# Optimization experiments

Hardware: AMD Instinct MI355X
Metric: run time of the kernel (lower is better)

Reference implementation:

```python
import jax, jax.numpy as jnp
import numpy as np

N_FALSE_NEG = 64
TEMPERATURE = 0.1
NORMALIZE = True

B, T, D = 32, 512, 512
M = 4096


def setup_inputs() -> dict:
    key = jax.random.key(0)
    k1, k2, k3 = jax.random.split(key, 3)
    input_predicted = jax.random.normal(k1, (B, T, D), dtype=jnp.float32)
    input_encoded = jax.random.normal(k2, (B, T, D), dtype=jnp.float32)
    rows = jax.random.randint(k3, (M,), 0, B)
    cols = jax.random.randint(jax.random.fold_in(k3, 1), (M,), 0, T)
    mask_ids = jnp.stack([rows, cols], axis=1).astype(jnp.int64)
    return {"input_predicted": input_predicted, "input_encoded": input_encoded, "mask_ids": mask_ids}


def _l2norm(x, eps=1e-12):
    # matches F.normalize(p=2, dim=-1)
    n = jnp.sqrt(jnp.sum(x * x, axis=-1, keepdims=True))
    return x / jnp.maximum(n, eps)


def reference(input_predicted, input_encoded, mask_ids):
    m = mask_ids.shape[0]
    rows, cols = mask_ids[:, 0], mask_ids[:, 1]
    enc = input_encoded[rows, cols]      # [M, D] encoded at masked positions
    preds = input_predicted[rows, cols]  # [M, D]

    # negatives_from_same_seq_only=False branch:
    # candidates = arange(0, M-1); idx_pos = i; torch.randint(0, M-2) -> [0, M-3]
    r = jax.random.randint(jax.random.key(42), (m, N_FALSE_NEG), 0, m - 2)  # [M, K]
    i = jnp.arange(m)[:, None]
    sel = r + (r >= i).astype(r.dtype)   # skip the positive index
    negatives = enc[sel]                 # [M, K, D]

    candidates = jnp.concatenate([enc[:, None, :], negatives], axis=1)  # [M, K+1, D]
    if NORMALIZE:
        candidates = _l2norm(candidates)
        preds = _l2norm(preds)

    sim = jnp.einsum('md,mcd->mc', preds, candidates) / TEMPERATURE  # [M, K+1]
    # cross entropy with target class 0
    lse = jax.nn.logsumexp(sim, axis=-1)
    loss = jnp.mean(lse - sim[:, 0])
    acc = jnp.mean((jnp.argmax(sim, axis=-1) == 0).astype(jnp.float32))
    return loss, acc
```

## Files before the change

kernel.cpp:

```cpp
#include <hip/hip_runtime.h>
#include <stdint.h>

#define T_DIM 512
#define D_DIM 512
#define M_ROWS 4096
#define NNEG 64
#define INV_TEMP 10.0f
#define SPAN 4094u
#define MULT 1024u

typedef float v2f __attribute__((ext_vector_type(2)));

struct U2 { uint32_t a, b; };

__host__ __device__ constexpr uint32_t rotl32(uint32_t x, uint32_t r) {
  return (x << r) | (x >> (32u - r));
}

__host__ __device__ constexpr U2 tf2x32(uint32_t k0, uint32_t k1,
                                        uint32_t c0, uint32_t c1) {
  uint32_t ks0 = k0, ks1 = k1, ks2 = k0 ^ k1 ^ 0x1BD11BDAu;
  uint32_t x0 = c0 + ks0, x1 = c1 + ks1;
  x0 += x1; x1 = rotl32(x1, 13); x1 ^= x0;
  x0 += x1; x1 = rotl32(x1, 15); x1 ^= x0;
  x0 += x1; x1 = rotl32(x1, 26); x1 ^= x0;
  x0 += x1; x1 = rotl32(x1, 6);  x1 ^= x0;
  x0 += ks1; x1 += ks2 + 1u;
  x0 += x1; x1 = rotl32(x1, 17); x1 ^= x0;
  x0 += x1; x1 = rotl32(x1, 29); x1 ^= x0;
  x0 += x1; x1 = rotl32(x1, 16); x1 ^= x0;
  x0 += x1; x1 = rotl32(x1, 24); x1 ^= x0;
  x0 += ks2; x1 += ks0 + 2u;
  x0 += x1; x1 = rotl32(x1, 13); x1 ^= x0;
  x0 += x1; x1 = rotl32(x1, 15); x1 ^= x0;
  x0 += x1; x1 = rotl32(x1, 26); x1 ^= x0;
  x0 += x1; x1 = rotl32(x1, 6);  x1 ^= x0;
  x0 += ks0; x1 += ks1 + 3u;
  x0 += x1; x1 = rotl32(x1, 17); x1 ^= x0;
  x0 += x1; x1 = rotl32(x1, 29); x1 ^= x0;
  x0 += x1; x1 = rotl32(x1, 16); x1 ^= x0;
  x0 += x1; x1 = rotl32(x1, 24); x1 ^= x0;
  x0 += ks1; x1 += ks2 + 4u;
  x0 += x1; x1 = rotl32(x1, 13); x1 ^= x0;
  x0 += x1; x1 = rotl32(x1, 15); x1 ^= x0;
  x0 += x1; x1 = rotl32(x1, 26); x1 ^= x0;
  x0 += x1; x1 = rotl32(x1, 6);  x1 ^= x0;
  x0 += ks2; x1 += ks0 + 5u;
  return U2{x0, x1};
}

constexpr U2 KHI = tf2x32(0u, 42u, 0u, 0u);
constexpr U2 KLO = tf2x32(0u, 42u, 0u, 1u);

__device__ inline uint32_t sel_index(uint32_t m, uint32_t j) {
  uint32_t pos = m * 64u + j;
  U2 h = tf2x32(KHI.a, KHI.b, 0u, pos);
  U2 l = tf2x32(KLO.a, KLO.b, 0u, pos);
  uint32_t hi = h.a ^ h.b;
  uint32_t lo = l.a ^ l.b;
  uint32_t r = ((hi % SPAN) * MULT + (lo % SPAN)) % SPAN;
  return r + (r >= m ? 1u : 0u);
}

__global__ __launch_bounds__(256) void k_norm_enc(
    const float* __restrict__ enc, const int* __restrict__ ids,
    int2* __restrict__ nenc) {
  int lane = threadIdx.x & 63;
  int wave = threadIdx.x >> 6;
  int m = blockIdx.x * 4 + wave;

  int2 rc = ((const int2*)ids)[m];
  size_t base = ((size_t)rc.x * T_DIM + rc.y) * D_DIM;
  const float4* ep = (const float4*)(enc + base);
  float4 e0 = ep[2 * lane], e1 = ep[2 * lane + 1];

  float se = e0.x*e0.x + e0.y*e0.y + e0.z*e0.z + e0.w*e0.w
           + e1.x*e1.x + e1.y*e1.y + e1.z*e1.z + e1.w*e1.w;
  #pragma unroll
  for (int off = 1; off < 64; off <<= 1) se += __shfl_xor(se, off, 64);
  float inv_e = 1.0f / fmaxf(sqrtf(se), 1e-12f);

  int w0 = __builtin_amdgcn_cvt_pk_fp8_f32(e0.x * inv_e, e0.y * inv_e, 0, false);
  w0     = __builtin_amdgcn_cvt_pk_fp8_f32(e0.z * inv_e, e0.w * inv_e, w0, true);
  int w1 = __builtin_amdgcn_cvt_pk_fp8_f32(e1.x * inv_e, e1.y * inv_e, 0, false);
  w1     = __builtin_amdgcn_cvt_pk_fp8_f32(e1.z * inv_e, e1.w * inv_e, w1, true);
  nenc[m * 64 + lane] = make_int2(w0, w1);
}

__device__ inline float dot8_fp8(int2 q, const float* pn) {
  v2f a = __builtin_amdgcn_cvt_pk_f32_fp8(q.x, false);
  float d = pn[0] * a.x;
  d = fmaf(pn[1], a.y, d);
  a = __builtin_amdgcn_cvt_pk_f32_fp8(q.x, true);
  d = fmaf(pn[2], a.x, d); d = fmaf(pn[3], a.y, d);
  a = __builtin_amdgcn_cvt_pk_f32_fp8(q.y, false);
  d = fmaf(pn[4], a.x, d); d = fmaf(pn[5], a.y, d);
  a = __builtin_amdgcn_cvt_pk_f32_fp8(q.y, true);
  d = fmaf(pn[6], a.x, d); d = fmaf(pn[7], a.y, d);
  return d;
}

__global__ __launch_bounds__(256) void k_contrast(
    const float* __restrict__ pred, const int* __restrict__ ids,
    const int2* __restrict__ nenc, float2* __restrict__ partials) {
  int lane = threadIdx.x & 63;
  int wave = threadIdx.x >> 6;
  int m = blockIdx.x * 4 + wave;

  __shared__ int sel_lds[4][64];
  __shared__ float2 wred[4];
  sel_lds[wave][lane] = (int)sel_index((uint32_t)m, (uint32_t)lane);

  int2 rc = ((const int2*)ids)[m];
  size_t base = ((size_t)rc.x * T_DIM + rc.y) * D_DIM;
  const float4* pp = (const float4*)(pred + base);
  float4 p0 = pp[2 * lane], p1 = pp[2 * lane + 1];
  float sp = p0.x*p0.x + p0.y*p0.y + p0.z*p0.z + p0.w*p0.w
           + p1.x*p1.x + p1.y*p1.y + p1.z*p1.z + p1.w*p1.w;
  #pragma unroll
  for (int off = 1; off < 64; off <<= 1) sp += __shfl_xor(sp, off, 64);
  float inv_p = 1.0f / fmaxf(sqrtf(sp), 1e-12f);

  float pn[8];
  pn[0] = p0.x*inv_p; pn[1] = p0.y*inv_p; pn[2] = p0.z*inv_p; pn[3] = p0.w*inv_p;
  pn[4] = p1.x*inv_p; pn[5] = p1.y*inv_p; pn[6] = p1.z*inv_p; pn[7] = p1.w*inv_p;

  float dp = dot8_fp8(nenc[m * 64 + lane], pn);
  #pragma unroll
  for (int off = 1; off < 64; off <<= 1) dp += __shfl_xor(dp, off, 64);
  float s0 = dp * INV_TEMP;

  float sumexp = __expf(s0);
  float maxneg = -1e30f;

  for (int jj = 0; jj < NNEG; jj += 4) {
    int4 s4 = *((const int4*)&sel_lds[wave][jj]);
    int2 q0 = nenc[(size_t)s4.x * 64 + lane];
    int2 q1 = nenc[(size_t)s4.y * 64 + lane];
    int2 q2 = nenc[(size_t)s4.z * 64 + lane];
    int2 q3 = nenc[(size_t)s4.w * 64 + lane];
    float d0 = dot8_fp8(q0, pn);
    float d1 = dot8_fp8(q1, pn);
    float d2 = dot8_fp8(q2, pn);
    float d3 = dot8_fp8(q3, pn);
    #pragma unroll
    for (int off = 1; off < 64; off <<= 1) {
      d0 += __shfl_xor(d0, off, 64);
      d1 += __shfl_xor(d1, off, 64);
      d2 += __shfl_xor(d2, off, 64);
      d3 += __shfl_xor(d3, off, 64);
    }
    float s_0 = d0 * INV_TEMP, s_1 = d1 * INV_TEMP;
    float s_2 = d2 * INV_TEMP, s_3 = d3 * INV_TEMP;
    maxneg = fmaxf(fmaxf(fmaxf(maxneg, s_0), fmaxf(s_1, s_2)), s_3);
    sumexp += __expf(s_0) + __expf(s_1) + __expf(s_2) + __expf(s_3);
  }

  if (lane == 0) {
    float lse = logf(sumexp);
    wred[wave] = make_float2(lse - s0, (s0 >= maxneg) ? 1.0f : 0.0f);
  }
  __syncthreads();
  if (threadIdx.x == 0) {
    float l = 0.0f, a = 0.0f;
    #pragma unroll
    for (int w = 0; w < 4; ++w) { l += wred[w].x; a += wred[w].y; }
    partials[blockIdx.x] = make_float2(l, a);
  }
}

__global__ __launch_bounds__(256) void k_finalize(
    const float2* __restrict__ partials, float* __restrict__ out) {
  int t = threadIdx.x;
  float l = 0.0f, a = 0.0f;
  #pragma unroll
  for (int i = 0; i < 4; ++i) {
    float2 v = partials[t + 256 * i];
    l += v.x; a += v.y;
  }
  #pragma unroll
  for (int off = 1; off < 64; off <<= 1) {
    l += __shfl_xor(l, off, 64);
    a += __shfl_xor(a, off, 64);
  }
  __shared__ float2 wred[4];
  if ((t & 63) == 0) wred[t >> 6] = make_float2(l, a);
  __syncthreads();
  if (t == 0) {
    out[0] = (wred[0].x + wred[1].x + wred[2].x + wred[3].x) * (1.0f / M_ROWS);
    out[1] = (wred[0].y + wred[1].y + wred[2].y + wred[3].y) * (1.0f / M_ROWS);
  }
}

extern "C" void kernel_launch(void* const* d_in, const int* in_sizes, int n_in,
                              void* d_out, int out_size, void* d_ws, size_t ws_size,
                              hipStream_t stream) {
  const float* pred = (const float*)d_in[0];
  const float* enc  = (const float*)d_in[1];
  const int*   ids  = (const int*)d_in[2];
  float* out = (float*)d_out;

  int2* nenc = (int2*)d_ws;
  float2* partials = (float2*)(nenc + (size_t)M_ROWS * 64);

  k_norm_enc<<<M_ROWS / 4, 256, 0, stream>>>(enc, ids, nenc);
  k_contrast<<<M_ROWS / 4, 256, 0, stream>>>(pred, ids, nenc, partials);
  k_finalize<<<1, 256, 0, stream>>>(partials, out);
}
```

Measured before the change: 115.1 us.

## Precompute negative indices, vectorize fp8 dots, quad-split reductions, fuse finalize via atomics

The Threefry negative-index generation moves into the normalization kernel and is written to a workspace table, so the contrast kernel only loads it. The fp8 dot product uses packed v2f FMAs. The per-negative 64-lane reductions are replaced by a scheme where four candidates share one butterfly, with each 16-lane quad finishing one candidate. The separate finalize kernel is removed: blocks accumulate float atomics and the last block writes the output. This removes one launch and cuts shuffle and hash ALU work, at the cost of nondeterministic float atomic ordering and a counter reset that depends on kernel ordering.

```diff
diff --git a/kernel.cpp b/kernel.cpp
--- a/kernel.cpp
+++ b/kernel.cpp
@@ -8,6 +8,7 @@
 #define INV_TEMP 10.0f
 #define SPAN 4094u
 #define MULT 1024u
+#define NBLK (M_ROWS / 4)
 
 typedef float v2f __attribute__((ext_vector_type(2)));
 
@@ -64,10 +65,15 @@
 
 __global__ __launch_bounds__(256) void k_norm_enc(
     const float* __restrict__ enc, const int* __restrict__ ids,
-    int2* __restrict__ nenc) {
+    int2* __restrict__ nenc, int* __restrict__ selTab,
+    unsigned int* __restrict__ accum) {
   int lane = threadIdx.x & 63;
   int wave = threadIdx.x >> 6;
   int m = blockIdx.x * 4 + wave;
+
+  if (blockIdx.x == 0 && threadIdx.x < 4) accum[threadIdx.x] = 0u;
+
+  selTab[m * 64 + lane] = (int)sel_index((uint32_t)m, (uint32_t)lane);
 
   int2 rc = ((const int2*)ids)[m];
   size_t base = ((size_t)rc.x * T_DIM + rc.y) * D_DIM;
@@ -87,29 +93,43 @@
   nenc[m * 64 + lane] = make_int2(w0, w1);
 }
 
-__device__ inline float dot8_fp8(int2 q, const float* pn) {
-  v2f a = __builtin_amdgcn_cvt_pk_f32_fp8(q.x, false);
-  float d = pn[0] * a.x;
-  d = fmaf(pn[1], a.y, d);
-  a = __builtin_amdgcn_cvt_pk_f32_fp8(q.x, true);
-  d = fmaf(pn[2], a.x, d); d = fmaf(pn[3], a.y, d);
-  a = __builtin_amdgcn_cvt_pk_f32_fp8(q.y, false);
-  d = fmaf(pn[4], a.x, d); d = fmaf(pn[5], a.y, d);
-  a = __builtin_amdgcn_cvt_pk_f32_fp8(q.y, true);
-  d = fmaf(pn[6], a.x, d); d = fmaf(pn[7], a.y, d);
-  return d;
+__device__ inline float dot8_fp8v(int2 q, const v2f* pn2) {
+  v2f a0 = __builtin_amdgcn_cvt_pk_f32_fp8(q.x, false);
+  v2f acc = a0 * pn2[0];
+  v2f a1 = __builtin_amdgcn_cvt_pk_f32_fp8(q.x, true);
+  acc = __builtin_elementwise_fma(a1, pn2[1], acc);
+  v2f a2 = __builtin_amdgcn_cvt_pk_f32_fp8(q.y, false);
+  acc = __builtin_elementwise_fma(a2, pn2[2], acc);
+  v2f a3 = __builtin_amdgcn_cvt_pk_f32_fp8(q.y, true);
+  acc = __builtin_elementwise_fma(a3, pn2[3], acc);
+  return acc.x + acc.y;
+}
+
+__device__ inline float reduce4(float d0, float d1, float d2, float d3, int quad) {
+  d0 += __shfl_xor(d0, 16, 64); d0 += __shfl_xor(d0, 32, 64);
+  d1 += __shfl_xor(d1, 16, 64); d1 += __shfl_xor(d1, 32, 64);
+  d2 += __shfl_xor(d2, 16, 64); d2 += __shfl_xor(d2, 32, 64);
+  d3 += __shfl_xor(d3, 16, 64); d3 += __shfl_xor(d3, 32, 64);
+  float c = (quad == 0) ? d0 : (quad == 1) ? d1 : (quad == 2) ? d2 : d3;
+  c += __shfl_xor(c, 1, 64);
+  c += __shfl_xor(c, 2, 64);
+  c += __shfl_xor(c, 4, 64);
+  c += __shfl_xor(c, 8, 64);
+  return c;
 }
 
 __global__ __launch_bounds__(256) void k_contrast(
     const float* __restrict__ pred, const int* __restrict__ ids,
-    const int2* __restrict__ nenc, float2* __restrict__ partials) {
+    const int2* __restrict__ nenc, const int* __restrict__ selTab,
+    unsigned int* __restrict__ accum, float* __restrict__ out) {
   int lane = threadIdx.x & 63;
   int wave = threadIdx.x >> 6;
   int m = blockIdx.x * 4 + wave;
+  int quad = lane >> 4;
 
   __shared__ int sel_lds[4][64];
   __shared__ float2 wred[4];
-  sel_lds[wave][lane] = (int)sel_index((uint32_t)m, (uint32_t)lane);
+  sel_lds[wave][lane] = selTab[m * 64 + lane];
 
   int2 rc = ((const int2*)ids)[m];
   size_t base = ((size_t)rc.x * T_DIM + rc.y) * D_DIM;
@@ -121,43 +141,47 @@
   for (int off = 1; off < 64; off <<= 1) sp += __shfl_xor(sp, off, 64);
   float inv_p = 1.0f / fmaxf(sqrtf(sp), 1e-12f);
 
-  float pn[8];
-  pn[0] = p0.x*inv_p; pn[1] = p0.y*inv_p; pn[2] = p0.z*inv_p; pn[3] = p0.w*inv_p;
-  pn[4] = p1.x*inv_p; pn[5] = p1.y*inv_p; pn[6] = p1.z*inv_p; pn[7] = p1.w*inv_p;
-
-  float dp = dot8_fp8(nenc[m * 64 + lane], pn);
+  v2f pn2[4];
+  pn2[0] = (v2f){p0.x * inv_p, p0.y * inv_p};
+  pn2[1] = (v2f){p0.z * inv_p, p0.w * inv_p};
+  pn2[2] = (v2f){p1.x * inv_p, p1.y * inv_p};
+  pn2[3] = (v2f){p1.z * inv_p, p1.w * inv_p};
+
+  float dp = dot8_fp8v(nenc[m * 64 + lane], pn2);
   #pragma unroll
   for (int off = 1; off < 64; off <<= 1) dp += __shfl_xor(dp, off, 64);
   float s0 = dp * INV_TEMP;
 
-  float sumexp = __expf(s0);
+  float sumexp_n = 0.0f;
   float maxneg = -1e30f;
 
-  for (int jj = 0; jj < NNEG; jj += 4) {
-    int4 s4 = *((const int4*)&sel_lds[wave][jj]);
-    int2 q0 = nenc[(size_t)s4.x * 64 + lane];
-    int2 q1 = nenc[(size_t)s4.y * 64 + lane];
-    int2 q2 = nenc[(size_t)s4.z * 64 + lane];
-    int2 q3 = nenc[(size_t)s4.w * 64 + lane];
-    float d0 = dot8_fp8(q0, pn);
-    float d1 = dot8_fp8(q1, pn);
-    float d2 = dot8_fp8(q2, pn);
-    float d3 = dot8_fp8(q3, pn);
-    #pragma unroll
-    for (int off = 1; off < 64; off <<= 1) {
-      d0 += __shfl_xor(d0, off, 64);
-      d1 += __shfl_xor(d1, off, 64);
-      d2 += __shfl_xor(d2, off, 64);
-      d3 += __shfl_xor(d3, off, 64);
-    }
-    float s_0 = d0 * INV_TEMP, s_1 = d1 * INV_TEMP;
-    float s_2 = d2 * INV_TEMP, s_3 = d3 * INV_TEMP;
-    maxneg = fmaxf(fmaxf(fmaxf(maxneg, s_0), fmaxf(s_1, s_2)), s_3);
-    sumexp += __expf(s_0) + __expf(s_1) + __expf(s_2) + __expf(s_3);
+  for (int jj = 0; jj < NNEG; jj += 8) {
+    int4 sa = *((const int4*)&sel_lds[wave][jj]);
+    int4 sb = *((const int4*)&sel_lds[wave][jj + 4]);
+    int2 q0 = nenc[(size_t)sa.x * 64 + lane];
+    int2 q1 = nenc[(size_t)sa.y * 64 + lane];
+    int2 q2 = nenc[(size_t)sa.z * 64 + lane];
+    int2 q3 = nenc[(size_t)sa.w * 64 + lane];
+    int2 q4 = nenc[(size_t)sb.x * 64 + lane];
+    int2 q5 = nenc[(size_t)sb.y * 64 + lane];
+    int2 q6 = nenc[(size_t)sb.z * 64 + lane];
+    int2 q7 = nenc[(size_t)sb.w * 64 + lane];
+    float d0 = dot8_fp8v(q0, pn2), d1 = dot8_fp8v(q1, pn2);
+    float d2 = dot8_fp8v(q2, pn2), d3 = dot8_fp8v(q3, pn2);
+    float d4 = dot8_fp8v(q4, pn2), d5 = dot8_fp8v(q5, pn2);
+    float d6 = dot8_fp8v(q6, pn2), d7 = dot8_fp8v(q7, pn2);
+    float c1 = reduce4(d0, d1, d2, d3, quad) * INV_TEMP;
+    float c2 = reduce4(d4, d5, d6, d7, quad) * INV_TEMP;
+    maxneg = fmaxf(maxneg, fmaxf(c1, c2));
+    sumexp_n += __expf(c1) + __expf(c2);
   }
+  sumexp_n += __shfl_xor(sumexp_n, 16, 64);
+  sumexp_n += __shfl_xor(sumexp_n, 32, 64);
+  maxneg = fmaxf(maxneg, __shfl_xor(maxneg, 16, 64));
+  maxneg = fmaxf(maxneg, __shfl_xor(maxneg, 32, 64));
 
   if (lane == 0) {
-    float lse = logf(sumexp);
+    float lse = logf(sumexp_n + __expf(s0));
     wred[wave] = make_float2(lse - s0, (s0 >= maxneg) ? 1.0f : 0.0f);
   }
   __syncthreads();
@@ -165,30 +189,17 @@
     float l = 0.0f, a = 0.0f;
     #pragma unroll
     for (int w = 0; w < 4; ++w) { l += wred[w].x; a += wred[w].y; }
-    partials[blockIdx.x] = make_float2(l, a);
-  }
-}
-
-__global__ __launch_bounds__(256) void k_finalize(
-    const float2* __restrict__ partials, float* __restrict__ out) {
-  int t = threadIdx.x;
-  float l = 0.0f, a = 0.0f;
-  #pragma unroll
-  for (int i = 0; i < 4; ++i) {
-    float2 v = partials[t + 256 * i];
-    l += v.x; a += v.y;
-  }
-  #pragma unroll
-  for (int off = 1; off < 64; off <<= 1) {
-    l += __shfl_xor(l, off, 64);
-    a += __shfl_xor(a, off, 64);
-  }
-  __shared__ float2 wred[4];
-  if ((t & 63) == 0) wred[t >> 6] = make_float2(l, a);
-  __syncthreads();
-  if (t == 0) {
-    out[0] = (wred[0].x + wred[1].x + wred[2].x + wred[3].x) * (1.0f / M_ROWS);
-    out[1] = (wred[0].y + wred[1].y + wred[2].y + wred[3].y) * (1.0f / M_ROWS);
+    float* facc = (float*)accum;
+    atomicAdd(&facc[0], l);
+    atomicAdd(&facc[1], a);
+    __threadfence();
+    unsigned int old = atomicAdd(&accum[2], 1u);
+    if (old == NBLK - 1) {
+      float ll = atomicAdd(&facc[0], 0.0f);
+      float aa = atomicAdd(&facc[1], 0.0f);
+      out[0] = ll * (1.0f / M_ROWS);
+      out[1] = aa * (1.0f / M_ROWS);
+    }
   }
 }
 
@@ -201,9 +212,9 @@
   float* out = (float*)d_out;
 
   int2* nenc = (int2*)d_ws;
-  float2* partials = (float2*)(nenc + (size_t)M_ROWS * 64);
-
-  k_norm_enc<<<M_ROWS / 4, 256, 0, stream>>>(enc, ids, nenc);
-  k_contrast<<<M_ROWS / 4, 256, 0, stream>>>(pred, ids, nenc, partials);
-  k_finalize<<<1, 256, 0, stream>>>(partials, out);
-}
+  int* selTab = (int*)(nenc + (size_t)M_ROWS * 64);
+  unsigned int* accum = (unsigned int*)(selTab + (size_t)M_ROWS * 64);
+
+  k_norm_enc<<<NBLK, 256, 0, stream>>>(enc, ids, nenc, selTab, accum);
+  k_contrast<<<NBLK, 256, 0, stream>>>(pred, ids, nenc, selTab, accum, out);
+}
```

Result: slower. 143.6 us (+24.7%).
